# Performance work log

Measured on AMD Instinct MI355X. Metric: run time of the kernel, lower is better.

Reference implementation:

```python
import jax, jax.numpy as jnp
import numpy as np

# NYU/Kinect 640x480 intrinsics from the source
FX = 582.6244816773795
FY = 582.6910327098864
CX = 313.0447587080473
CY = 238.44389626620386
EPS = 1e-07


def setup_inputs() -> dict:
    key = jax.random.key(0)
    k1, k2 = jax.random.split(key)
    B, C, H, W = 64, 1, 480, 640
    fake = jax.random.uniform(k1, (B, C, H, W), dtype=jnp.float32)
    real = jax.random.uniform(k2, (B, C, H, W), dtype=jnp.float32)
    return {"fake": fake, "real": real}


def _xyz(depth, col, row):
    # point_cloud() followed by *1000: the /1000 inside and *1000 outside cancel.
    z = depth                      # [B,C,H,W]
    x = depth * (col - CX) / FX
    y = depth * (row - CY) / FY
    # pcd[pcd == 0] = eps
    z = jnp.where(z == 0.0, EPS, z)
    x = jnp.where(x == 0.0, EPS, x)
    y = jnp.where(y == 0.0, EPS, y)
    return x, y, z


def _masked_rmse(a, b, mask, n):
    d = jnp.where(mask, a - b, 0.0)
    return jnp.sqrt(jnp.sum(d * d) / n)


def reference(fake, real):
    H, W = real.shape[-2], real.shape[-1]
    col = jnp.arange(W, dtype=jnp.float32)            # broadcast over last dim
    row = jnp.arange(H, dtype=jnp.float32)[:, None]   # broadcast over rows

    valid_r = (real > 0.0) & (real < 1.0)
    valid_f = (fake > 0.0) & (fake < 1.0)
    # Original compacts real-valid first, then fake-valid: net mask is the AND.
    mask = valid_r & valid_f
    n = jnp.sum(mask.astype(jnp.float32))

    xr, yr, zr = _xyz(real, col, row)
    xf, yf, zf = _xyz(fake, col, row)

    lossX = _masked_rmse(xr, xf, mask, n)
    lossY = _masked_rmse(yr, yf, mask, n)
    lossZ = _masked_rmse(zr, zf, mask, n)

    log_zr = jnp.log(jnp.abs(jnp.where(mask, zr, 1.0)))
    log_zf = jnp.log(jnp.abs(jnp.where(mask, zf, 1.0)))
    rmse_log = _masked_rmse(log_zr, log_zf, mask, n)

    loss = 10.0 * (rmse_log + jnp.abs(10.0 * (3.0 - jnp.exp(lossX) - jnp.exp(lossY) - jnp.exp(lossZ))))
    return loss
```

## Files before the change

### kernel.cpp

```cpp
#include <hip/hip_runtime.h>
#include <math.h>

#define NBLOCKS 1280
#define NTHREADS 256
#define THREADS_TOTAL (NBLOCKS * NTHREADS)
#define ITERS 15

#define ROW4 160
#define IMG4 76800

#define K_CX 313.0447587080473f
#define K_CY 238.44389626620386f
#define K_RFX (1.0f / 582.6244816773795f)
#define K_RFY (1.0f / 582.6910327098864f)
#define LN2_SQ 0.48045301391820142467f

__device__ __forceinline__ void quad_accum(const float4& f, const float4& r,
                                           int col4, float b,
                                           float& sx, float& sy, float& sz,
                                           float& sl2, float& cnt) {
    float fv[4] = {f.x, f.y, f.z, f.w};
    float rv[4] = {r.x, r.y, r.z, r.w};
#pragma unroll
    for (int j = 0; j < 4; ++j) {
        float fj = fv[j], rj = rv[j];
        bool m = (rj > 0.f) & (rj < 1.f) & (fj > 0.f) & (fj < 1.f);
        float a  = ((float)(col4 + j) - K_CX) * K_RFX;
        float d  = rj - fj;
        float dl = __log2f(rj) - __log2f(fj);
        d  = m ? d  : 0.f;
        dl = m ? dl : 0.f;
        float da = d * a, db = d * b;
        sx  += da * da;
        sy  += db * db;
        sz  += d * d;
        sl2 += dl * dl;
        cnt += m ? 1.f : 0.f;
    }
}

__device__ __forceinline__ void block_reduce_store(
        float cnt, float sx, float sy, float sz, float sl,
        double* __restrict__ partial, int nb, int bid) {
#pragma unroll
    for (int o = 32; o > 0; o >>= 1) {
        cnt += __shfl_down(cnt, o);
        sx  += __shfl_down(sx, o);
        sy  += __shfl_down(sy, o);
        sz  += __shfl_down(sz, o);
        sl  += __shfl_down(sl, o);
    }
    __shared__ float part[4][5];
    int wave = threadIdx.x >> 6;
    int lane = threadIdx.x & 63;
    if (lane == 0) {
        part[wave][0] = cnt; part[wave][1] = sx; part[wave][2] = sy;
        part[wave][3] = sz;  part[wave][4] = sl;
    }
    __syncthreads();
    if (threadIdx.x == 0) {
        double t[5] = {0, 0, 0, 0, 0};
#pragma unroll
        for (int w = 0; w < 4; ++w)
#pragma unroll
            for (int j = 0; j < 5; ++j) t[j] += (double)part[w][j];
#pragma unroll
        for (int j = 0; j < 5; ++j) partial[j * nb + bid] = t[j];
    }
}

__global__ __launch_bounds__(NTHREADS) void ddd_reduce15_kernel(
        const float4* __restrict__ fake, const float4* __restrict__ real,
        double* __restrict__ partial) {
    const int tid = blockIdx.x * NTHREADS + threadIdx.x;

    float cnt = 0.f, sx = 0.f, sy = 0.f, sz = 0.f, sl2 = 0.f;

    float4 fb[ITERS], rb[ITERS];
#pragma unroll
    for (int k = 0; k < ITERS; ++k) {
        fb[k] = fake[tid + k * THREADS_TOTAL];
        rb[k] = real[tid + k * THREADS_TOTAL];
    }

#pragma unroll
    for (int k = 0; k < ITERS; ++k) {
        int idx  = tid + k * THREADS_TOTAL;
        int pos  = idx % IMG4;
        int col4 = (pos % ROW4) * 4;
        int h    = pos / ROW4;
        float b  = ((float)h - K_CY) * K_RFY;
        quad_accum(fb[k], rb[k], col4, b, sx, sy, sz, sl2, cnt);
    }

    block_reduce_store(cnt, sx, sy, sz, sl2 * LN2_SQ, partial, NBLOCKS, blockIdx.x);
}

__global__ __launch_bounds__(NTHREADS) void ddd_reduce_gen_kernel(
        const float4* __restrict__ fake, const float4* __restrict__ real,
        double* __restrict__ partial, int total4) {
    float cnt = 0.f, sx = 0.f, sy = 0.f, sz = 0.f, sl2 = 0.f;
    for (int i = blockIdx.x * NTHREADS + threadIdx.x; i < total4; i += THREADS_TOTAL) {
        float4 f = fake[i];
        float4 r = real[i];
        int pos  = i % IMG4;
        int col4 = (pos % ROW4) * 4;
        int h    = pos / ROW4;
        float b  = ((float)h - K_CY) * K_RFY;
        quad_accum(f, r, col4, b, sx, sy, sz, sl2, cnt);
    }
    block_reduce_store(cnt, sx, sy, sz, sl2 * LN2_SQ, partial, NBLOCKS, blockIdx.x);
}

__global__ __launch_bounds__(NTHREADS) void finalize_kernel(
        const double* __restrict__ partial, int nb, float* __restrict__ out) {
    double t[5] = {0, 0, 0, 0, 0};
    for (int i = threadIdx.x; i < nb; i += NTHREADS)
#pragma unroll
        for (int j = 0; j < 5; ++j) t[j] += partial[j * nb + i];
#pragma unroll
    for (int o = 32; o > 0; o >>= 1)
#pragma unroll
        for (int j = 0; j < 5; ++j) t[j] += __shfl_down(t[j], o);

    __shared__ double part[4][5];
    int wave = threadIdx.x >> 6;
    int lane = threadIdx.x & 63;
    if (lane == 0)
#pragma unroll
        for (int j = 0; j < 5; ++j) part[wave][j] = t[j];
    __syncthreads();

    if (threadIdx.x == 0) {
#pragma unroll
        for (int w = 1; w < 4; ++w)
#pragma unroll
            for (int j = 0; j < 5; ++j) part[0][j] += part[w][j];
        double n  = part[0][0];
        double lx = sqrt(part[0][1] / n);
        double ly = sqrt(part[0][2] / n);
        double lz = sqrt(part[0][3] / n);
        double ll = sqrt(part[0][4] / n);
        double loss = 10.0 * (ll + fabs(10.0 * (3.0 - exp(lx) - exp(ly) - exp(lz))));
        out[0] = (float)loss;
    }
}

extern "C" void kernel_launch(void* const* d_in, const int* in_sizes, int n_in,
                              void* d_out, int out_size, void* d_ws, size_t ws_size,
                              hipStream_t stream) {
    const float4* fake = (const float4*)d_in[0];
    const float4* real = (const float4*)d_in[1];
    float* out = (float*)d_out;
    double* partial = (double*)d_ws;

    int total  = in_sizes[0];
    int total4 = total / 4;

    if (total4 == ITERS * THREADS_TOTAL) {
        ddd_reduce15_kernel<<<NBLOCKS, NTHREADS, 0, stream>>>(fake, real, partial);
    } else {
        ddd_reduce_gen_kernel<<<NBLOCKS, NTHREADS, 0, stream>>>(fake, real, partial, total4);
    }
    finalize_kernel<<<1, NTHREADS, 0, stream>>>(partial, NBLOCKS, out);
}
```

Baseline: 36.02 us.

## Fuse finalize into reduction via last-block atomic counter and hoist column factors

Removes the separate finalize kernel launch by having the last block to finish, detected with an atomic counter and thread fences, perform the final double-precision reduction and loss computation. A memset launch is added to reset the counter. Also hoists per-column x factors out of the loop by accumulating per-lane d² and applying a² once at the end. The row index is advanced incrementally instead of being recomputed with div/mod. The atomic-and-fence handshake adds a serialised tail to the last block, and the memset adds its own launch.

Measured after the change: 78.23 us. +117.2%, slower.

```diff
diff --git a/kernel.cpp b/kernel.cpp
--- a/kernel.cpp
+++ b/kernel.cpp
@@ -8,6 +8,7 @@
 
 #define ROW4 160
 #define IMG4 76800
+#define H_STEP 128
 
 #define K_CX 313.0447587080473f
 #define K_CY 238.44389626620386f
@@ -15,33 +16,8 @@
 #define K_RFY (1.0f / 582.6910327098864f)
 #define LN2_SQ 0.48045301391820142467f
 
-__device__ __forceinline__ void quad_accum(const float4& f, const float4& r,
-                                           int col4, float b,
-                                           float& sx, float& sy, float& sz,
-                                           float& sl2, float& cnt) {
-    float fv[4] = {f.x, f.y, f.z, f.w};
-    float rv[4] = {r.x, r.y, r.z, r.w};
-#pragma unroll
-    for (int j = 0; j < 4; ++j) {
-        float fj = fv[j], rj = rv[j];
-        bool m = (rj > 0.f) & (rj < 1.f) & (fj > 0.f) & (fj < 1.f);
-        float a  = ((float)(col4 + j) - K_CX) * K_RFX;
-        float d  = rj - fj;
-        float dl = __log2f(rj) - __log2f(fj);
-        d  = m ? d  : 0.f;
-        dl = m ? dl : 0.f;
-        float da = d * a, db = d * b;
-        sx  += da * da;
-        sy  += db * db;
-        sz  += d * d;
-        sl2 += dl * dl;
-        cnt += m ? 1.f : 0.f;
-    }
-}
-
-__device__ __forceinline__ void block_reduce_store(
-        float cnt, float sx, float sy, float sz, float sl,
-        double* __restrict__ partial, int nb, int bid) {
+__device__ __forceinline__ void block_reduce(
+        float cnt, float sx, float sy, float sz, float sl, double t[5]) {
 #pragma unroll
     for (int o = 32; o > 0; o >>= 1) {
         cnt += __shfl_down(cnt, o);
@@ -59,22 +35,76 @@
     }
     __syncthreads();
     if (threadIdx.x == 0) {
-        double t[5] = {0, 0, 0, 0, 0};
+#pragma unroll
+        for (int j = 0; j < 5; ++j) t[j] = 0.0;
 #pragma unroll
         for (int w = 0; w < 4; ++w)
 #pragma unroll
             for (int j = 0; j < 5; ++j) t[j] += (double)part[w][j];
+    }
+}
+
+__device__ __forceinline__ void store_and_finalize(
+        const double t[5], double* __restrict__ partial, unsigned* __restrict__ counter,
+        int nb, int bid, float* __restrict__ out) {
+    __shared__ int lastFlag;
+    if (threadIdx.x == 0) {
 #pragma unroll
         for (int j = 0; j < 5; ++j) partial[j * nb + bid] = t[j];
+        __threadfence();
+        unsigned old = atomicAdd(counter, 1u);
+        lastFlag = (old == (unsigned)(nb - 1));
+    }
+    __syncthreads();
+    if (!lastFlag) return;
+
+    __threadfence();
+    double s[5] = {0, 0, 0, 0, 0};
+    for (int i = threadIdx.x; i < nb; i += NTHREADS)
+#pragma unroll
+        for (int j = 0; j < 5; ++j) s[j] += partial[j * nb + i];
+#pragma unroll
+    for (int o = 32; o > 0; o >>= 1)
+#pragma unroll
+        for (int j = 0; j < 5; ++j) s[j] += __shfl_down(s[j], o);
+
+    __shared__ double dpart[4][5];
+    int wave = threadIdx.x >> 6;
+    int lane = threadIdx.x & 63;
+    if (lane == 0)
+#pragma unroll
+        for (int j = 0; j < 5; ++j) dpart[wave][j] = s[j];
+    __syncthreads();
+    if (threadIdx.x == 0) {
+#pragma unroll
+        for (int w = 1; w < 4; ++w)
+#pragma unroll
+            for (int j = 0; j < 5; ++j) dpart[0][j] += dpart[w][j];
+        double n  = dpart[0][0];
+        double lx = sqrt(dpart[0][1] / n);
+        double ly = sqrt(dpart[0][2] / n);
+        double lz = sqrt(dpart[0][3] / n);
+        double ll = sqrt(dpart[0][4] / n);
+        double loss = 10.0 * (ll + fabs(10.0 * (3.0 - exp(lx) - exp(ly) - exp(lz))));
+        out[0] = (float)loss;
     }
 }
 
 __global__ __launch_bounds__(NTHREADS) void ddd_reduce15_kernel(
         const float4* __restrict__ fake, const float4* __restrict__ real,
-        double* __restrict__ partial) {
-    const int tid = blockIdx.x * NTHREADS + threadIdx.x;
-
-    float cnt = 0.f, sx = 0.f, sy = 0.f, sz = 0.f, sl2 = 0.f;
+        double* __restrict__ partial, unsigned* __restrict__ counter,
+        float* __restrict__ out) {
+    const int tid  = blockIdx.x * NTHREADS + threadIdx.x;
+    const int pos  = tid % IMG4;
+    const int col4 = (pos % ROW4) * 4;
+    int h          = pos / ROW4;
+
+    float a2v[4];
+#pragma unroll
+    for (int j = 0; j < 4; ++j) {
+        float a = ((float)(col4 + j) - K_CX) * K_RFX;
+        a2v[j] = a * a;
+    }
 
     float4 fb[ITERS], rb[ITERS];
 #pragma unroll
@@ -83,67 +113,72 @@
         rb[k] = real[tid + k * THREADS_TOTAL];
     }
 
+    float cnt = 0.f, sy = 0.f, sl2 = 0.f;
+    float sd2[4] = {0.f, 0.f, 0.f, 0.f};
 #pragma unroll
     for (int k = 0; k < ITERS; ++k) {
-        int idx  = tid + k * THREADS_TOTAL;
-        int pos  = idx % IMG4;
-        int col4 = (pos % ROW4) * 4;
-        int h    = pos / ROW4;
-        float b  = ((float)h - K_CY) * K_RFY;
-        quad_accum(fb[k], rb[k], col4, b, sx, sy, sz, sl2, cnt);
-    }
-
-    block_reduce_store(cnt, sx, sy, sz, sl2 * LN2_SQ, partial, NBLOCKS, blockIdx.x);
+        float b = ((float)h - K_CY) * K_RFY;
+        h += H_STEP; if (h >= 480) h -= 480;
+        float fv[4] = {fb[k].x, fb[k].y, fb[k].z, fb[k].w};
+        float rv[4] = {rb[k].x, rb[k].y, rb[k].z, rb[k].w};
+#pragma unroll
+        for (int j = 0; j < 4; ++j) {
+            float fj = fv[j], rj = rv[j];
+            bool m = (rj > 0.f) & (rj < 1.f) & (fj > 0.f) & (fj < 1.f);
+            float d  = rj - fj;
+            float dl = __log2f(rj) - __log2f(fj);
+            d  = m ? d  : 0.f;
+            dl = m ? dl : 0.f;
+            float db = d * b;
+            sd2[j] += d * d;
+            sy     += db * db;
+            sl2    += dl * dl;
+            cnt    += m ? 1.f : 0.f;
+        }
+    }
+
+    float sz = sd2[0] + sd2[1] + sd2[2] + sd2[3];
+    float sx = a2v[0]*sd2[0] + a2v[1]*sd2[1] + a2v[2]*sd2[2] + a2v[3]*sd2[3];
+
+    double t[5];
+    block_reduce(cnt, sx, sy, sz, sl2 * LN2_SQ, t);
+    store_and_finalize(t, partial, counter, NBLOCKS, blockIdx.x, out);
 }
 
 __global__ __launch_bounds__(NTHREADS) void ddd_reduce_gen_kernel(
         const float4* __restrict__ fake, const float4* __restrict__ real,
-        double* __restrict__ partial, int total4) {
+        double* __restrict__ partial, unsigned* __restrict__ counter,
+        float* __restrict__ out, int total4) {
     float cnt = 0.f, sx = 0.f, sy = 0.f, sz = 0.f, sl2 = 0.f;
     for (int i = blockIdx.x * NTHREADS + threadIdx.x; i < total4; i += THREADS_TOTAL) {
         float4 f = fake[i];
         float4 r = real[i];
         int pos  = i % IMG4;
         int col4 = (pos % ROW4) * 4;
-        int h    = pos / ROW4;
-        float b  = ((float)h - K_CY) * K_RFY;
-        quad_accum(f, r, col4, b, sx, sy, sz, sl2, cnt);
-    }
-    block_reduce_store(cnt, sx, sy, sz, sl2 * LN2_SQ, partial, NBLOCKS, blockIdx.x);
-}
-
-__global__ __launch_bounds__(NTHREADS) void finalize_kernel(
-        const double* __restrict__ partial, int nb, float* __restrict__ out) {
-    double t[5] = {0, 0, 0, 0, 0};
-    for (int i = threadIdx.x; i < nb; i += NTHREADS)
-#pragma unroll
-        for (int j = 0; j < 5; ++j) t[j] += partial[j * nb + i];
-#pragma unroll
-    for (int o = 32; o > 0; o >>= 1)
-#pragma unroll
-        for (int j = 0; j < 5; ++j) t[j] += __shfl_down(t[j], o);
-
-    __shared__ double part[4][5];
-    int wave = threadIdx.x >> 6;
-    int lane = threadIdx.x & 63;
-    if (lane == 0)
-#pragma unroll
-        for (int j = 0; j < 5; ++j) part[wave][j] = t[j];
-    __syncthreads();
-
-    if (threadIdx.x == 0) {
-#pragma unroll
-        for (int w = 1; w < 4; ++w)
-#pragma unroll
-            for (int j = 0; j < 5; ++j) part[0][j] += part[w][j];
-        double n  = part[0][0];
-        double lx = sqrt(part[0][1] / n);
-        double ly = sqrt(part[0][2] / n);
-        double lz = sqrt(part[0][3] / n);
-        double ll = sqrt(part[0][4] / n);
-        double loss = 10.0 * (ll + fabs(10.0 * (3.0 - exp(lx) - exp(ly) - exp(lz))));
-        out[0] = (float)loss;
-    }
+        int hh   = pos / ROW4;
+        float b  = ((float)hh - K_CY) * K_RFY;
+        float fv[4] = {f.x, f.y, f.z, f.w};
+        float rv[4] = {r.x, r.y, r.z, r.w};
+#pragma unroll
+        for (int j = 0; j < 4; ++j) {
+            float fj = fv[j], rj = rv[j];
+            bool m = (rj > 0.f) & (rj < 1.f) & (fj > 0.f) & (fj < 1.f);
+            float a  = ((float)(col4 + j) - K_CX) * K_RFX;
+            float d  = rj - fj;
+            float dl = __log2f(rj) - __log2f(fj);
+            d  = m ? d  : 0.f;
+            dl = m ? dl : 0.f;
+            float da = d * a, db = d * b;
+            sx  += da * da;
+            sy  += db * db;
+            sz  += d * d;
+            sl2 += dl * dl;
+            cnt += m ? 1.f : 0.f;
+        }
+    }
+    double t[5];
+    block_reduce(cnt, sx, sy, sz, sl2 * LN2_SQ, t);
+    store_and_finalize(t, partial, counter, NBLOCKS, blockIdx.x, out);
 }
 
 extern "C" void kernel_launch(void* const* d_in, const int* in_sizes, int n_in,
@@ -153,14 +188,17 @@
     const float4* real = (const float4*)d_in[1];
     float* out = (float*)d_out;
     double* partial = (double*)d_ws;
+    unsigned* counter = (unsigned*)((char*)d_ws + 5 * NBLOCKS * sizeof(double));
 
     int total  = in_sizes[0];
     int total4 = total / 4;
 
+    hipMemsetAsync(counter, 0, sizeof(unsigned), stream);
     if (total4 == ITERS * THREADS_TOTAL) {
-        ddd_reduce15_kernel<<<NBLOCKS, NTHREADS, 0, stream>>>(fake, real, partial);
+        ddd_reduce15_kernel<<<NBLOCKS, NTHREADS, 0, stream>>>(
+            fake, real, partial, counter, out);
     } else {
-        ddd_reduce_gen_kernel<<<NBLOCKS, NTHREADS, 0, stream>>>(fake, real, partial, total4);
-    }
-    finalize_kernel<<<1, NTHREADS, 0, stream>>>(partial, NBLOCKS, out);
-}
+        ddd_reduce_gen_kernel<<<NBLOCKS, NTHREADS, 0, stream>>>(
+            fake, real, partial, counter, out, total4);
+    }
+}
```
